# Kernel optimization log

Measured on AMD Instinct MI355X. Metric: run time of the kernel, lower is better.

Reference implementation:

```python
import jax, jax.numpy as jnp
import numpy as np

N_USERS = 50000
N_ITEMS = 75000
N_NODES = N_USERS + N_ITEMS
NNZ = 1250000
EMB = 64
N_LAYERS = 3
BATCH = 4096
EPS = 1e-12


def setup_inputs() -> dict:
    key = jax.random.key(0)
    ks = jax.random.split(key, 12)
    xavier = float(np.sqrt(6.0 / (EMB + EMB)))
    return {
        "user": jax.random.randint(ks[0], (BATCH,), 0, N_USERS, dtype=jnp.int64 if jax.config.jax_enable_x64 else jnp.int32),
        "pos_item": jax.random.randint(ks[1], (BATCH,), 0, N_ITEMS, dtype=jnp.int32),
        "neg_item": jax.random.randint(ks[2], (BATCH,), 0, N_ITEMS, dtype=jnp.int32),
        "row": jax.random.randint(ks[3], (NNZ,), 0, N_NODES, dtype=jnp.int32),
        "col": jax.random.randint(ks[4], (NNZ,), 0, N_NODES, dtype=jnp.int32),
        "vals": jax.random.uniform(ks[5], (NNZ,), dtype=jnp.float32),
        "emb": jax.random.normal(ks[6], (N_NODES, EMB), dtype=jnp.float32) * 0.1,
        "W1": jax.random.uniform(ks[7], (N_LAYERS, EMB, EMB), minval=-xavier, maxval=xavier, dtype=jnp.float32),
        "b1": jnp.zeros((N_LAYERS, EMB), dtype=jnp.float32),
        "W2": jax.random.uniform(ks[8], (N_LAYERS, EMB, EMB), minval=-xavier, maxval=xavier, dtype=jnp.float32),
        "b2": jnp.zeros((N_LAYERS, EMB), dtype=jnp.float32),
    }


def _l2_normalize(x):
    n = jnp.linalg.norm(x, axis=-1, keepdims=True)
    return x / jnp.maximum(n, EPS)


def reference(user, pos_item, neg_item, row, col, vals, emb, W1, b1, W2, b2):
    # eval mode: node_dropout / mess_dropout inactive (rates 0)
    node_feat = emb
    all_embeddings = [node_feat]
    for l in range(N_LAYERS):
        # sparse SpMM: agg[i] = sum_j A[i,j] * node_feat[j]
        msg = vals[:, None] * node_feat[col]            # [nnz, d]
        agg = jax.ops.segment_sum(msg, row, num_segments=N_NODES)  # [N, d]
        part_1 = jax.nn.leaky_relu(agg @ W1[l].T + b1[l], 0.2)
        part_2 = jax.nn.leaky_relu((agg * node_feat) @ W2[l].T + b2[l], 0.2)
        node_feat = part_1 + part_2
        all_embeddings.append(_l2_normalize(node_feat))
    embedding_weight = jnp.concatenate(all_embeddings, axis=-1)  # [N, 4*d]
    gcn_user = embedding_weight[:N_USERS]
    gcn_item = embedding_weight[N_USERS:]
    return (gcn_user[user], gcn_item[pos_item], gcn_item[neg_item])
```

## Files before the change

### kernel.cpp

```cpp
#include <hip/hip_runtime.h>
#include <hip/hip_fp16.h>

#define N_USERS 50000
#define N_ITEMS 75000
#define N_NODES 125000
#define N_PAD   125008
#define NNZ     1250000
#define EMB     64
#define N_LAYERS 3
#define BATCH   4096
#define CONCAT  256

#define BROWS   128
#define NB      ((N_NODES + BROWS - 1) / BROWS)
#define CHUNK   4096
#define NCHUNK  ((NNZ + CHUNK - 1) / CHUNK)
#define EPT     (CHUNK / 256)
#define BCAP    1600
#define FB_NODES 32

typedef _Float16 half8  __attribute__((ext_vector_type(8)));
typedef float    floatx4 __attribute__((ext_vector_type(4)));

__device__ __forceinline__ bool user_is_i64(const void* uptr) {
    const int* u = (const int*)uptr;
    return (u[1] | u[3] | u[5] | u[7]) == 0;
}
__device__ __forceinline__ int load_user(const void* uptr, int b, bool is64) {
    return is64 ? (int)((const long long*)uptr)[b] : ((const int*)uptr)[b];
}
__device__ __forceinline__ int sample_node(const void* user, const int* pos,
                                           const int* neg, int which, int b,
                                           bool is64) {
    if (which == 0) return load_user(user, b, is64);
    return N_USERS + (which == 1 ? pos[b] : neg[b]);
}

__device__ __forceinline__ float unpack_val(unsigned w) {
    unsigned short us = (unsigned short)(w >> 17);
    _Float16 h = __builtin_bit_cast(_Float16, us);
    return (float)h;
}

__global__ void init_kernel(const float* __restrict__ emb,
                            _Float16* __restrict__ f16,
                            const void* __restrict__ user,
                            const int* __restrict__ pos,
                            const int* __restrict__ neg,
                            float* __restrict__ out) {
    int i = blockIdx.x * 256 + threadIdx.x;
    if (i < N_NODES * EMB) {
        f16[i] = (_Float16)emb[i];
    } else {
        int j = i - N_NODES * EMB;
        if (j < 3 * BATCH * EMB) {
            bool is64 = user_is_i64(user);
            int which = j / (BATCH * EMB);
            int rem   = j % (BATCH * EMB);
            int b = rem >> 6, d = rem & 63;
            int node = sample_node(user, pos, neg, which, b, is64);
            out[(which * BATCH + b) * CONCAT + d] = emb[node * EMB + d];
        }
    }
}

__global__ __launch_bounds__(256) void partition_kernel(
    const int* __restrict__ row, const int* __restrict__ col,
    const float* __restrict__ vals, int* __restrict__ bcnt,
    unsigned long long* __restrict__ sw8) {
    __shared__ int h[NB];
    __shared__ int base[NB];
    int t = threadIdx.x;
    int e0 = blockIdx.x * CHUNK;
    int e1 = e0 + CHUNK; if (e1 > NNZ) e1 = NNZ;
    for (int i = t; i < NB; i += 256) h[i] = 0;
    __syncthreads();

    unsigned long long rec[EPT];
    int bkt[EPT];
    int pos[EPT];
    int cnt = 0;
    for (int e = e0 + t; e < e1; e += 256) {
        int r = row[e];
        int b = r >> 7;
        _Float16 hv = (_Float16)vals[e];
        unsigned hb = (unsigned)__builtin_bit_cast(unsigned short, hv);
        rec[cnt] = ((unsigned long long)hb << 24)
                 | ((unsigned)(r & 127) << 17)
                 | (unsigned)col[e];
        bkt[cnt] = b;
        pos[cnt] = atomicAdd(&h[b], 1);
        ++cnt;
    }
    __syncthreads();
    for (int i = t; i < NB; i += 256) {
        int c = h[i];
        if (c) base[i] = atomicAdd(&bcnt[i], c);
    }
    __syncthreads();
    for (int k = 0; k < cnt; ++k) {
        int b = bkt[k];
        sw8[(size_t)b * BCAP + base[b] + pos[k]] = rec[k];
    }
}

__global__ __launch_bounds__(256) void bucket_sort_kernel(
    const int* __restrict__ bcnt,
    const unsigned long long* __restrict__ sw8,
    unsigned* __restrict__ se, int* __restrict__ off, int* __restrict__ endv) {
    __shared__ unsigned long long ew[BCAP];
    __shared__ unsigned eo[BCAP];
    __shared__ int rh[BROWS], rb[BROWS], rc[BROWS];
    __shared__ int s[256];

    int b = blockIdx.x, t = threadIdx.x;
    int n = bcnt[b];
    int s0 = b * BCAP;
    if (t < BROWS) rh[t] = 0;
    __syncthreads();
    const unsigned long long* src = sw8 + (size_t)b * BCAP;
    for (int i = t; i < n; i += 256) {
        unsigned long long rec = src[i];
        ew[i] = rec;
        atomicAdd(&rh[(int)((rec >> 17) & 127)], 1);
    }
    __syncthreads();
    s[t] = (t < BROWS) ? rh[t] : 0;
    __syncthreads();
    for (int d = 1; d < 256; d <<= 1) {
        int x = (t >= d) ? s[t - d] : 0;
        __syncthreads();
        s[t] += x;
        __syncthreads();
    }
    if (t < BROWS) {
        int excl = s[t] - rh[t];
        rb[t] = excl;
        rc[t] = 0;
        int r = b * BROWS + t;
        if (r < N_NODES) {
            off[r]  = s0 + excl;
            endv[r] = s0 + s[t];
        }
    }
    __syncthreads();
    for (int i = t; i < n; i += 256) {
        unsigned long long rec = ew[i];
        int r = (int)((rec >> 17) & 127);
        int p = rb[r] + atomicAdd(&rc[r], 1);
        eo[p] = (unsigned)(((rec >> 24) << 17) | (rec & 0x1FFFFULL));
    }
    __syncthreads();
    for (int i = t; i < n; i += 256)
        se[(size_t)s0 + i] = eo[i];
}

__global__ __launch_bounds__(256) void layer_kernel(
    const int* __restrict__ off, const int* __restrict__ endv,
    const unsigned* __restrict__ se,
    const _Float16* __restrict__ fin, _Float16* __restrict__ fout,
    const float* __restrict__ W1, const float* __restrict__ b1,
    const float* __restrict__ W2, const float* __restrict__ b2, int layer) {

    __shared__ _Float16 wlds[2][EMB][EMB];
    __shared__ _Float16 alds[FB_NODES][EMB];

    int tid = threadIdx.x;

    {
        const float* Wsrc0 = W1 + layer * EMB * EMB;
        const float* Wsrc1 = W2 + layer * EMB * EMB;
        #pragma unroll
        for (int m = 0; m < 2; ++m) {
            const float* Ws = m ? Wsrc1 : Wsrc0;
            for (int c = tid; c < 512; c += 256) {
                int n = c >> 3, c16 = c & 7;
                const float* p = Ws + n * EMB + c16 * 8;
                floatx4 wa = *(const floatx4*)p, wb = *(const floatx4*)(p + 4);
                half8 h;
                #pragma unroll
                for (int i = 0; i < 4; ++i) {
                    h[i] = (_Float16)wa[i]; h[4 + i] = (_Float16)wb[i];
                }
                *(half8*)(&wlds[m][n][(c16 ^ (n & 7)) * 8]) = h;
            }
        }
    }

    int wave = tid >> 6, lane = tid & 63;
    int g = lane >> 3;
    int k = lane & 7;
    int base = blockIdx.x * FB_NODES;
    int ln = wave * 8 + g;
    int node = base + ln;
    bool valid = node < N_NODES;

    int j   = valid ? off[node]  : 0;
    int end = valid ? endv[node] : 0;

    float acc[8] = {0.f, 0.f, 0.f, 0.f, 0.f, 0.f, 0.f, 0.f};
    const _Float16* fink = fin + k * 8;

    while (__any(j < end)) {
        unsigned ev[4];
        #pragma unroll
        for (int t = 0; t < 4; ++t)
            ev[t] = (j + t < end) ? se[j + t] : 0u;
        half8 h[4];
        #pragma unroll
        for (int t = 0; t < 4; ++t) {
            int c = (int)(ev[t] & 0x1FFFFu);
            h[t] = *(const half8*)(fink + (size_t)c * EMB);
        }
        #pragma unroll
        for (int t = 0; t < 4; ++t) {
            float val = unpack_val(ev[t]);
            #pragma unroll
            for (int i = 0; i < 8; ++i)
                acc[i] += (float)h[t][i] * val;
        }
        j += 4;
    }

    {
        half8 o;
        #pragma unroll
        for (int i = 0; i < 8; ++i) o[i] = (_Float16)acc[i];
        *(half8*)(&alds[ln][(k ^ (ln & 7)) * 8]) = o;
    }
    __syncthreads();

    if (wave < 2) {
        int lm = lane & 15, quad = lane >> 4;
        int ln0 = wave * 16 + lm;
        int nb = base + wave * 16;
        int nodeD = nb + lm;
        int sw = lm & 7;

        half8 a0 = *(const half8*)(&alds[ln0][(quad ^ sw) * 8]);
        half8 a1 = *(const half8*)(&alds[ln0][((quad + 4) ^ sw) * 8]);

        int nsafe = nodeD < N_NODES ? nodeD : 0;
        const half8* fp = (const half8*)(fin + (size_t)nsafe * EMB + quad * 8);
        half8 f0 = fp[0], f1 = fp[4];
        half8 g0 = a0 * f0, g1 = a1 * f1;

        #pragma unroll
        for (int t = 0; t < 4; ++t) {
            int n = t * 16 + lm;
            float bias1 = b1[layer * EMB + n];
            float bias2 = b2[layer * EMB + n];
            half8 w10 = *(const half8*)(&wlds[0][n][(quad ^ sw) * 8]);
            half8 w11 = *(const half8*)(&wlds[0][n][((quad + 4) ^ sw) * 8]);
            half8 w20 = *(const half8*)(&wlds[1][n][(quad ^ sw) * 8]);
            half8 w21 = *(const half8*)(&wlds[1][n][((quad + 4) ^ sw) * 8]);
            floatx4 d1 = {0.f, 0.f, 0.f, 0.f}, d2 = {0.f, 0.f, 0.f, 0.f};
            d1 = __builtin_amdgcn_mfma_f32_16x16x32_f16(a0, w10, d1, 0, 0, 0);
            d1 = __builtin_amdgcn_mfma_f32_16x16x32_f16(a1, w11, d1, 0, 0, 0);
            d2 = __builtin_amdgcn_mfma_f32_16x16x32_f16(g0, w20, d2, 0, 0, 0);
            d2 = __builtin_amdgcn_mfma_f32_16x16x32_f16(g1, w21, d2, 0, 0, 0);
            int dim = t * 16 + lm;
            #pragma unroll
            for (int r = 0; r < 4; ++r) {
                int nodeO = nb + quad * 4 + r;
                float p1v = d1[r] + bias1;
                p1v = p1v > 0.f ? p1v : 0.2f * p1v;
                float p2v = d2[r] + bias2;
                p2v = p2v > 0.f ? p2v : 0.2f * p2v;
                float nf = p1v + p2v;
                if (nodeO < N_NODES)
                    fout[(size_t)nodeO * EMB + dim] = (_Float16)nf;
            }
        }
    }
}

__global__ __launch_bounds__(256) void gatherL_kernel(
    const void* __restrict__ user, const int* __restrict__ pos,
    const int* __restrict__ neg, const _Float16* __restrict__ feat,
    float* __restrict__ out, int layer) {

    int w = blockIdx.x * 4 + (threadIdx.x >> 6);
    int lane = threadIdx.x & 63;
    if (w >= 3 * BATCH) return;
    bool is64 = user_is_i64(user);
    int which = w / BATCH, b = w % BATCH;
    int node = sample_node(user, pos, neg, which, b, is64);

    float f = (float)feat[(size_t)node * EMB + lane];
    float sq = f * f;
    #pragma unroll
    for (int off = 32; off; off >>= 1) sq += __shfl_xor(sq, off, 64);
    float norm = fmaxf(sqrtf(sq), 1e-12f);

    out[w * CONCAT + (layer + 1) * EMB + lane] = f / norm;
}

extern "C" void kernel_launch(void* const* d_in, const int* in_sizes, int n_in,
                              void* d_out, int out_size, void* d_ws, size_t ws_size,
                              hipStream_t stream) {
    const void* user = d_in[0];
    const int* pos  = (const int*)d_in[1];
    const int* neg  = (const int*)d_in[2];
    const int* row  = (const int*)d_in[3];
    const int* col  = (const int*)d_in[4];
    const float* vals = (const float*)d_in[5];
    const float* emb  = (const float*)d_in[6];
    const float* W1   = (const float*)d_in[7];
    const float* b1   = (const float*)d_in[8];
    const float* W2   = (const float*)d_in[9];
    const float* b2   = (const float*)d_in[10];

    _Float16* f16a   = (_Float16*)d_ws;
    _Float16* f16b   = f16a + (size_t)N_PAD * EMB;
    int*      off    = (int*)(f16b + (size_t)N_PAD * EMB);
    int*      endv   = off + (N_NODES + 8);
    int*      bcnt   = endv + (N_NODES + 8);
    unsigned long long* sw8 = (unsigned long long*)(bcnt + 984);
    unsigned* se     = (unsigned*)(sw8 + (size_t)NB * BCAP);

    float* out = (float*)d_out;

    hipMemsetAsync(bcnt, 0, (size_t)NB * sizeof(int), stream);
    partition_kernel<<<NCHUNK, 256, 0, stream>>>(row, col, vals, bcnt, sw8);
    bucket_sort_kernel<<<NB, 256, 0, stream>>>(bcnt, sw8, se, off, endv);

    init_kernel<<<(N_NODES * EMB + 3 * BATCH * EMB + 255) / 256, 256, 0, stream>>>(
        emb, f16a, user, pos, neg, out);

    const _Float16* fin = f16a;
    _Float16* fout = f16b;
    for (int l = 0; l < N_LAYERS; ++l) {
        layer_kernel<<<(N_NODES + FB_NODES - 1) / FB_NODES, 256, 0, stream>>>(
            off, endv, se, fin, fout, W1, b1, W2, b2, l);
        gatherL_kernel<<<(3 * BATCH + 3) / 4, 256, 0, stream>>>(
            user, pos, neg, fout, out, l);
        const _Float16* tmp = fout; fout = (_Float16*)fin; fin = (const _Float16*)tmp;
    }
}
```

Measured before the change: 273.7 us.

## Fuse preprocessing into one cooperative kernel and fold gather-normalize into layer kernel

The memset, partition, bucket-sort and init kernels are merged into one cooperative prep kernel with grid syncs, with partition chunks resized so one block per bucket covers all edges. The per-layer gather/normalize kernel is removed: each layer kernel computes the L2 norm of its output rows and scatters normalized rows directly to the output through a node-to-sample map built in prep. The SpMM inner loop is unrolled to 8 edges, and the last layer skips writing its feature buffer. This cuts launch count and a pass over features, at the cost of grid-sync overhead, extra register pressure, and a sample map capped at 8 duplicates per node.

Measured after the change: 503.2 us. 83.8% more time.

```diff
diff --git a/kernel.cpp b/kernel.cpp
--- a/kernel.cpp
+++ b/kernel.cpp
@@ -1,5 +1,6 @@
 #include <hip/hip_runtime.h>
 #include <hip/hip_fp16.h>
+#include <hip/hip_cooperative_groups.h>
 
 #define N_USERS 50000
 #define N_ITEMS 75000
@@ -13,11 +14,11 @@
 
 #define BROWS   128
 #define NB      ((N_NODES + BROWS - 1) / BROWS)
-#define CHUNK   4096
-#define NCHUNK  ((NNZ + CHUNK - 1) / CHUNK)
-#define EPT     (CHUNK / 256)
+#define PCHUNK  1280
+#define PEPT    (PCHUNK / 256)
 #define BCAP    1600
 #define FB_NODES 32
+#define SCAP    8
 
 typedef _Float16 half8  __attribute__((ext_vector_type(8)));
 typedef float    floatx4 __attribute__((ext_vector_type(4)));
@@ -42,117 +43,126 @@
     return (float)h;
 }
 
-__global__ void init_kernel(const float* __restrict__ emb,
-                            _Float16* __restrict__ f16,
-                            const void* __restrict__ user,
-                            const int* __restrict__ pos,
-                            const int* __restrict__ neg,
-                            float* __restrict__ out) {
-    int i = blockIdx.x * 256 + threadIdx.x;
-    if (i < N_NODES * EMB) {
-        f16[i] = (_Float16)emb[i];
-    } else {
-        int j = i - N_NODES * EMB;
-        if (j < 3 * BATCH * EMB) {
-            bool is64 = user_is_i64(user);
-            int which = j / (BATCH * EMB);
-            int rem   = j % (BATCH * EMB);
-            int b = rem >> 6, d = rem & 63;
-            int node = sample_node(user, pos, neg, which, b, is64);
-            out[(which * BATCH + b) * CONCAT + d] = emb[node * EMB + d];
-        }
-    }
-}
-
-__global__ __launch_bounds__(256) void partition_kernel(
+__global__ __launch_bounds__(256) void prep_kernel(
     const int* __restrict__ row, const int* __restrict__ col,
-    const float* __restrict__ vals, int* __restrict__ bcnt,
-    unsigned long long* __restrict__ sw8) {
-    __shared__ int h[NB];
-    __shared__ int base[NB];
-    int t = threadIdx.x;
-    int e0 = blockIdx.x * CHUNK;
-    int e1 = e0 + CHUNK; if (e1 > NNZ) e1 = NNZ;
-    for (int i = t; i < NB; i += 256) h[i] = 0;
-    __syncthreads();
-
-    unsigned long long rec[EPT];
-    int bkt[EPT];
-    int pos[EPT];
-    int cnt = 0;
-    for (int e = e0 + t; e < e1; e += 256) {
-        int r = row[e];
-        int b = r >> 7;
-        _Float16 hv = (_Float16)vals[e];
-        unsigned hb = (unsigned)__builtin_bit_cast(unsigned short, hv);
-        rec[cnt] = ((unsigned long long)hb << 24)
-                 | ((unsigned)(r & 127) << 17)
-                 | (unsigned)col[e];
-        bkt[cnt] = b;
-        pos[cnt] = atomicAdd(&h[b], 1);
-        ++cnt;
-    }
-    __syncthreads();
-    for (int i = t; i < NB; i += 256) {
-        int c = h[i];
-        if (c) base[i] = atomicAdd(&bcnt[i], c);
-    }
-    __syncthreads();
-    for (int k = 0; k < cnt; ++k) {
-        int b = bkt[k];
-        sw8[(size_t)b * BCAP + base[b] + pos[k]] = rec[k];
-    }
-}
-
-__global__ __launch_bounds__(256) void bucket_sort_kernel(
-    const int* __restrict__ bcnt,
-    const unsigned long long* __restrict__ sw8,
-    unsigned* __restrict__ se, int* __restrict__ off, int* __restrict__ endv) {
-    __shared__ unsigned long long ew[BCAP];
+    const float* __restrict__ vals, const float* __restrict__ emb,
+    const void* __restrict__ user, const int* __restrict__ pos,
+    const int* __restrict__ neg,
+    _Float16* __restrict__ f16, float* __restrict__ out,
+    int* __restrict__ bcnt, int* __restrict__ scnt, int* __restrict__ smap,
+    unsigned long long* __restrict__ sw8, unsigned* __restrict__ se,
+    int* __restrict__ off, int* __restrict__ endv) {
+
+    __shared__ union {
+        struct { int h[NB]; int base[NB]; } p;
+        unsigned long long ew[BCAP];
+    } u;
     __shared__ unsigned eo[BCAP];
     __shared__ int rh[BROWS], rb[BROWS], rc[BROWS];
     __shared__ int s[256];
 
-    int b = blockIdx.x, t = threadIdx.x;
-    int n = bcnt[b];
-    int s0 = b * BCAP;
-    if (t < BROWS) rh[t] = 0;
-    __syncthreads();
-    const unsigned long long* src = sw8 + (size_t)b * BCAP;
-    for (int i = t; i < n; i += 256) {
-        unsigned long long rec = src[i];
-        ew[i] = rec;
-        atomicAdd(&rh[(int)((rec >> 17) & 127)], 1);
-    }
-    __syncthreads();
-    s[t] = (t < BROWS) ? rh[t] : 0;
-    __syncthreads();
-    for (int d = 1; d < 256; d <<= 1) {
-        int x = (t >= d) ? s[t - d] : 0;
-        __syncthreads();
-        s[t] += x;
-        __syncthreads();
-    }
-    if (t < BROWS) {
-        int excl = s[t] - rh[t];
-        rb[t] = excl;
-        rc[t] = 0;
-        int r = b * BROWS + t;
-        if (r < N_NODES) {
-            off[r]  = s0 + excl;
-            endv[r] = s0 + s[t];
-        }
-    }
-    __syncthreads();
-    for (int i = t; i < n; i += 256) {
-        unsigned long long rec = ew[i];
-        int r = (int)((rec >> 17) & 127);
-        int p = rb[r] + atomicAdd(&rc[r], 1);
-        eo[p] = (unsigned)(((rec >> 24) << 17) | (rec & 0x1FFFFULL));
-    }
-    __syncthreads();
-    for (int i = t; i < n; i += 256)
-        se[(size_t)s0 + i] = eo[i];
+    cooperative_groups::grid_group grid = cooperative_groups::this_grid();
+    const int t = threadIdx.x, b = blockIdx.x;
+    const int gid = b * 256 + t;
+    const int gsz = NB * 256;
+    const bool is64 = user_is_i64(user);
+
+    for (int i = gid; i < NB; i += gsz) bcnt[i] = 0;
+    for (int i = gid; i < N_NODES; i += gsz) scnt[i] = 0;
+    for (int i = gid; i < N_NODES * EMB + 3 * BATCH * EMB; i += gsz) {
+        if (i < N_NODES * EMB) {
+            f16[i] = (_Float16)emb[i];
+        } else {
+            int j = i - N_NODES * EMB;
+            int which = j / (BATCH * EMB);
+            int rem   = j % (BATCH * EMB);
+            int bb = rem >> 6, d = rem & 63;
+            int node = sample_node(user, pos, neg, which, bb, is64);
+            out[(which * BATCH + bb) * CONCAT + d] = emb[node * EMB + d];
+        }
+    }
+    grid.sync();
+
+    if (gid < 3 * BATCH) {
+        int which = gid / BATCH, bb = gid % BATCH;
+        int node = sample_node(user, pos, neg, which, bb, is64);
+        int slot = atomicAdd(&scnt[node], 1);
+        if (slot < SCAP) smap[node * SCAP + slot] = gid;
+    }
+    {
+        int e0 = b * PCHUNK;
+        int e1 = e0 + PCHUNK; if (e1 > NNZ) e1 = NNZ;
+        for (int i = t; i < NB; i += 256) u.p.h[i] = 0;
+        __syncthreads();
+        unsigned long long rec[PEPT];
+        int bkt[PEPT], ps[PEPT];
+        int cnt = 0;
+        for (int e = e0 + t; e < e1; e += 256) {
+            int r = row[e];
+            int bk = r >> 7;
+            _Float16 hv = (_Float16)vals[e];
+            unsigned hb = (unsigned)__builtin_bit_cast(unsigned short, hv);
+            rec[cnt] = ((unsigned long long)hb << 24)
+                     | ((unsigned)(r & 127) << 17)
+                     | (unsigned)col[e];
+            bkt[cnt] = bk;
+            ps[cnt] = atomicAdd(&u.p.h[bk], 1);
+            ++cnt;
+        }
+        __syncthreads();
+        for (int i = t; i < NB; i += 256) {
+            int c = u.p.h[i];
+            if (c) u.p.base[i] = atomicAdd(&bcnt[i], c);
+        }
+        __syncthreads();
+        for (int k = 0; k < cnt; ++k) {
+            int bk = bkt[k];
+            sw8[(size_t)bk * BCAP + u.p.base[bk] + ps[k]] = rec[k];
+        }
+    }
+    grid.sync();
+
+    {
+        int n = bcnt[b];
+        int s0 = b * BCAP;
+        if (t < BROWS) rh[t] = 0;
+        __syncthreads();
+        const unsigned long long* src = sw8 + (size_t)b * BCAP;
+        for (int i = t; i < n; i += 256) {
+            unsigned long long rec = src[i];
+            u.ew[i] = rec;
+            atomicAdd(&rh[(int)((rec >> 17) & 127)], 1);
+        }
+        __syncthreads();
+        s[t] = (t < BROWS) ? rh[t] : 0;
+        __syncthreads();
+        for (int d = 1; d < 256; d <<= 1) {
+            int x = (t >= d) ? s[t - d] : 0;
+            __syncthreads();
+            s[t] += x;
+            __syncthreads();
+        }
+        if (t < BROWS) {
+            int excl = s[t] - rh[t];
+            rb[t] = excl;
+            rc[t] = 0;
+            int r = b * BROWS + t;
+            if (r < N_NODES) {
+                off[r]  = s0 + excl;
+                endv[r] = s0 + s[t];
+            }
+        }
+        __syncthreads();
+        for (int i = t; i < n; i += 256) {
+            unsigned long long rec = u.ew[i];
+            int r = (int)((rec >> 17) & 127);
+            int p = rb[r] + atomicAdd(&rc[r], 1);
+            eo[p] = (unsigned)(((rec >> 24) << 17) | (rec & 0x1FFFFULL));
+        }
+        __syncthreads();
+        for (int i = t; i < n; i += 256)
+            se[(size_t)s0 + i] = eo[i];
+    }
 }
 
 __global__ __launch_bounds__(256) void layer_kernel(
@@ -160,7 +170,9 @@
     const unsigned* __restrict__ se,
     const _Float16* __restrict__ fin, _Float16* __restrict__ fout,
     const float* __restrict__ W1, const float* __restrict__ b1,
-    const float* __restrict__ W2, const float* __restrict__ b2, int layer) {
+    const float* __restrict__ W2, const float* __restrict__ b2,
+    const int* __restrict__ scnt, const int* __restrict__ smap,
+    float* __restrict__ out, int layer) {
 
     __shared__ _Float16 wlds[2][EMB][EMB];
     __shared__ _Float16 alds[FB_NODES][EMB];
@@ -202,24 +214,24 @@
     const _Float16* fink = fin + k * 8;
 
     while (__any(j < end)) {
-        unsigned ev[4];
-        #pragma unroll
-        for (int t = 0; t < 4; ++t)
+        unsigned ev[8];
+        #pragma unroll
+        for (int t = 0; t < 8; ++t)
             ev[t] = (j + t < end) ? se[j + t] : 0u;
-        half8 h[4];
-        #pragma unroll
-        for (int t = 0; t < 4; ++t) {
+        half8 h[8];
+        #pragma unroll
+        for (int t = 0; t < 8; ++t) {
             int c = (int)(ev[t] & 0x1FFFFu);
             h[t] = *(const half8*)(fink + (size_t)c * EMB);
         }
         #pragma unroll
-        for (int t = 0; t < 4; ++t) {
+        for (int t = 0; t < 8; ++t) {
             float val = unpack_val(ev[t]);
             #pragma unroll
             for (int i = 0; i < 8; ++i)
                 acc[i] += (float)h[t][i] * val;
         }
-        j += 4;
+        j += 8;
     }
 
     {
@@ -244,6 +256,9 @@
         const half8* fp = (const half8*)(fin + (size_t)nsafe * EMB + quad * 8);
         half8 f0 = fp[0], f1 = fp[4];
         half8 g0 = a0 * f0, g1 = a1 * f1;
+
+        float nfv[4][4];
+        float sq[4] = {0.f, 0.f, 0.f, 0.f};
 
         #pragma unroll
         for (int t = 0; t < 4; ++t) {
@@ -268,32 +283,36 @@
                 float p2v = d2[r] + bias2;
                 p2v = p2v > 0.f ? p2v : 0.2f * p2v;
                 float nf = p1v + p2v;
-                if (nodeO < N_NODES)
+                nfv[t][r] = nf;
+                sq[r] += nf * nf;
+                if (layer != N_LAYERS - 1 && nodeO < N_NODES)
                     fout[(size_t)nodeO * EMB + dim] = (_Float16)nf;
             }
         }
-    }
-}
-
-__global__ __launch_bounds__(256) void gatherL_kernel(
-    const void* __restrict__ user, const int* __restrict__ pos,
-    const int* __restrict__ neg, const _Float16* __restrict__ feat,
-    float* __restrict__ out, int layer) {
-
-    int w = blockIdx.x * 4 + (threadIdx.x >> 6);
-    int lane = threadIdx.x & 63;
-    if (w >= 3 * BATCH) return;
-    bool is64 = user_is_i64(user);
-    int which = w / BATCH, b = w % BATCH;
-    int node = sample_node(user, pos, neg, which, b, is64);
-
-    float f = (float)feat[(size_t)node * EMB + lane];
-    float sq = f * f;
-    #pragma unroll
-    for (int off = 32; off; off >>= 1) sq += __shfl_xor(sq, off, 64);
-    float norm = fmaxf(sqrtf(sq), 1e-12f);
-
-    out[w * CONCAT + (layer + 1) * EMB + lane] = f / norm;
+
+        #pragma unroll
+        for (int r = 0; r < 4; ++r) {
+            float v = sq[r];
+            #pragma unroll
+            for (int m = 1; m < 16; m <<= 1) v += __shfl_xor(v, m, 64);
+            sq[r] = fmaxf(sqrtf(v), 1e-12f);
+        }
+
+        #pragma unroll
+        for (int r = 0; r < 4; ++r) {
+            int nodeO = nb + quad * 4 + r;
+            if (nodeO >= N_NODES) continue;
+            int c = scnt[nodeO]; c = c < SCAP ? c : SCAP;
+            float inv = 1.0f / sq[r];
+            for (int i2 = 0; i2 < c; ++i2) {
+                int smp = smap[nodeO * SCAP + i2];
+                float* po = out + (size_t)smp * CONCAT + (layer + 1) * EMB;
+                #pragma unroll
+                for (int t = 0; t < 4; ++t)
+                    po[t * 16 + lm] = nfv[t][r] * inv;
+            }
+        }
+    }
 }
 
 extern "C" void kernel_launch(void* const* d_in, const int* in_sizes, int n_in,
@@ -316,25 +335,30 @@
     int*      off    = (int*)(f16b + (size_t)N_PAD * EMB);
     int*      endv   = off + (N_NODES + 8);
     int*      bcnt   = endv + (N_NODES + 8);
-    unsigned long long* sw8 = (unsigned long long*)(bcnt + 984);
+    int*      scnt   = bcnt + 984;
+    int*      smap   = scnt + N_NODES;
+    unsigned long long* sw8 = (unsigned long long*)(smap + N_NODES * SCAP);
     unsigned* se     = (unsigned*)(sw8 + (size_t)NB * BCAP);
 
     float* out = (float*)d_out;
 
-    hipMemsetAsync(bcnt, 0, (size_t)NB * sizeof(int), stream);
-    partition_kernel<<<NCHUNK, 256, 0, stream>>>(row, col, vals, bcnt, sw8);
-    bucket_sort_kernel<<<NB, 256, 0, stream>>>(bcnt, sw8, se, off, endv);
-
-    init_kernel<<<(N_NODES * EMB + 3 * BATCH * EMB + 255) / 256, 256, 0, stream>>>(
-        emb, f16a, user, pos, neg, out);
+    {
+        void* args[] = {
+            (void*)&row, (void*)&col, (void*)&vals, (void*)&emb,
+            (void*)&user, (void*)&pos, (void*)&neg,
+            (void*)&f16a, (void*)&out,
+            (void*)&bcnt, (void*)&scnt, (void*)&smap,
+            (void*)&sw8, (void*)&se, (void*)&off, (void*)&endv
+        };
+        hipLaunchCooperativeKernel((const void*)prep_kernel, dim3(NB), dim3(256),
+                                   args, 0, stream);
+    }
 
     const _Float16* fin = f16a;
     _Float16* fout = f16b;
     for (int l = 0; l < N_LAYERS; ++l) {
         layer_kernel<<<(N_NODES + FB_NODES - 1) / FB_NODES, 256, 0, stream>>>(
-            off, endv, se, fin, fout, W1, b1, W2, b2, l);
-        gatherL_kernel<<<(3 * BATCH + 3) / 4, 256, 0, stream>>>(
-            user, pos, neg, fout, out, l);
+            off, endv, se, fin, fout, W1, b1, W2, b2, scnt, smap, out, l);
         const _Float16* tmp = fout; fout = (_Float16*)fin; fin = (const _Float16*)tmp;
     }
 }
```
